# Kernel optimization log

Measured on AMD Instinct MI355X. Metric: run time of the kernel, lower is better.

The kernel has to match this reference:

```python
import jax, jax.numpy as jnp
import numpy as np


def setup_inputs() -> dict:
    key = jax.random.key(0)
    k1, k2 = jax.random.split(key)
    B, C, N = 8, 64, 65536
    features = jax.random.normal(k1, (B, C, N), dtype=jnp.float32)
    coords = jax.random.uniform(k2, (B, 3, N), dtype=jnp.float32)  # normalized xyz in [0,1)
    return {"features": features, "coords": coords, "resolution": 32}


def reference(features, coords, resolution):
    """avg_voxelize: quantize coords to an r^3 grid, scatter-average features.

    features: [B, C, N] float; coords: [B, 3, N] float in [0,1].
    Returns (vox [B, C, r, r, r], norm_coords [B, 3, N]).
    """
    r = resolution
    B, C, N = features.shape
    norm_coords = jnp.clip(coords * r, 0, r - 1)                 # [B, 3, N]
    vox = jnp.round(norm_coords).astype(jnp.int32)               # [B, 3, N]
    # linear voxel index per point: x*r^2 + y*r + z
    idx = (vox[:, 0] * r + vox[:, 1]) * r + vox[:, 2]            # [B, N]
    flat_idx = (idx + jnp.arange(B, dtype=jnp.int32)[:, None] * (r * r * r)).reshape(-1)  # [B*N]
    feats = features.transpose(0, 2, 1).reshape(B * N, C)        # [B*N, C]
    num_seg = B * r * r * r
    sums = jax.ops.segment_sum(feats, flat_idx, num_segments=num_seg)            # [B*r^3, C]
    cnt = jax.ops.segment_sum(jnp.ones((B * N,), features.dtype), flat_idx,
                              num_segments=num_seg)                              # [B*r^3]
    avg = sums / jnp.maximum(cnt, 1.0)[:, None]
    out = avg.reshape(B, r, r, r, C).transpose(0, 4, 1, 2, 3)    # [B, C, r, r, r]
    return out, norm_coords
```

## Files before the change

### kernel.cpp

```cpp
#include <hip/hip_runtime.h>
#include <hip/hip_bf16.h>


#define BB 8
#define CC 64
#define NN 65536
#define RR 32
#define R3 (RR * RR * RR)
#define OFFSTRIDE (R3 + 1)

__global__ __launch_bounds__(256) void points_kernel(
    const float* __restrict__ coords,
    float* __restrict__ norm_out,
    unsigned int* __restrict__ cnt,
    unsigned int* __restrict__ packed)
{
    int gid = blockIdx.x * 256 + threadIdx.x;
    int b = gid >> 16;
    int n = gid & (NN - 1);

    const float* cb = coords + (size_t)b * 3 * NN;
    float x = cb[n];
    float y = cb[NN + n];
    float z = cb[2 * NN + n];

    float nx = fminf(fmaxf(x * (float)RR, 0.0f), (float)(RR - 1));
    float ny = fminf(fmaxf(y * (float)RR, 0.0f), (float)(RR - 1));
    float nz = fminf(fmaxf(z * (float)RR, 0.0f), (float)(RR - 1));

    float* nb = norm_out + (size_t)b * 3 * NN;
    nb[n] = nx;
    nb[NN + n] = ny;
    nb[2 * NN + n] = nz;

    int vx = (int)rintf(nx);
    int vy = (int)rintf(ny);
    int vz = (int)rintf(nz);
    unsigned int idx = (unsigned int)((vx * RR + vy) * RR + vz);

    unsigned int rank = atomicAdd(&cnt[b * R3 + idx], 1u);
    packed[gid] = (idx << 17) | rank;
}

__global__ __launch_bounds__(1024) void scan_kernel(
    const unsigned int* __restrict__ cnt,
    unsigned int* __restrict__ off)
{
    int b = blockIdx.x;
    int t = threadIdx.x;
    const unsigned int* c = cnt + (size_t)b * R3;
    unsigned int* o = off + (size_t)b * OFFSTRIDE;

    unsigned int loc[32];
    unsigned int s = 0;
    #pragma unroll
    for (int k = 0; k < 32; k++) { loc[k] = c[t * 32 + k]; s += loc[k]; }

    __shared__ unsigned int aux[1024];
    aux[t] = s;
    __syncthreads();
    for (int d = 1; d < 1024; d <<= 1) {
        unsigned int v = (t >= d) ? aux[t - d] : 0u;
        __syncthreads();
        aux[t] += v;
        __syncthreads();
    }
    unsigned int run = (t == 0) ? 0u : aux[t - 1];
    #pragma unroll
    for (int k = 0; k < 32; k++) { o[t * 32 + k] = run; run += loc[k]; }
    if (t == 1023) o[R3] = run;
}

__global__ __launch_bounds__(256) void pos_kernel(
    const unsigned int* __restrict__ packed,
    const unsigned int* __restrict__ off,
    unsigned int* __restrict__ pos)
{
    int gid = blockIdx.x * 256 + threadIdx.x;
    int b = gid >> 16;
    unsigned int pk = packed[gid];
    unsigned int ix = pk >> 17;
    unsigned int rk = pk & 0x1FFFFu;
    pos[gid] = off[(size_t)b * OFFSTRIDE + ix] + rk;
}

__global__ __launch_bounds__(1024) void gather_kernel(
    const float* __restrict__ feats,
    const unsigned int* __restrict__ pos,
    const unsigned int* __restrict__ off,
    float* __restrict__ out)
{
    __shared__ __hip_bfloat16 srt[NN];

    int c = blockIdx.x;
    int b = blockIdx.y;
    int t = threadIdx.x;

    const float* f = feats + ((size_t)b * CC + c) * NN;
    const unsigned int* P = pos + (size_t)b * NN;

    for (int n0 = t * 4; n0 < NN; n0 += 1024 * 4) {
        float4 fv = *(const float4*)(f + n0);
        uint4 pv = *(const uint4*)(P + n0);
        srt[pv.x] = __float2bfloat16(fv.x);
        srt[pv.y] = __float2bfloat16(fv.y);
        srt[pv.z] = __float2bfloat16(fv.z);
        srt[pv.w] = __float2bfloat16(fv.w);
    }
    __syncthreads();

    const unsigned int* O = off + (size_t)b * OFFSTRIDE;
    float* ob = out + ((size_t)b * CC + c) * R3;
    for (int j = 0; j < 32; j++) {
        int v = t + j * 1024;
        unsigned int s0 = O[v];
        unsigned int s1 = O[v + 1];
        float s = 0.0f;
        for (unsigned int p = s0; p < s1; p++) s += __bfloat162float(srt[p]);
        float cf = (float)(s1 - s0);
        ob[v] = s / fmaxf(cf, 1.0f);
    }
}

extern "C" void kernel_launch(void* const* d_in, const int* in_sizes, int n_in,
                              void* d_out, int out_size, void* d_ws, size_t ws_size,
                              hipStream_t stream) {
    const float* feats  = (const float*)d_in[0];
    const float* coords = (const float*)d_in[1];

    float* out_vox  = (float*)d_out;
    float* out_norm = out_vox + (size_t)BB * CC * R3;

    char* ws = (char*)d_ws;
    unsigned int* cnt    = (unsigned int*)ws;
    unsigned int* off    = (unsigned int*)(ws + 1048576);
    unsigned int* packed = (unsigned int*)(ws + 1048576 + 1048608);
    unsigned int* pos    = (unsigned int*)(ws + 1048576 + 1048608 + 2097152);

    hipMemsetAsync(cnt, 0, (size_t)BB * R3 * sizeof(unsigned int), stream);

    points_kernel<<<(BB * NN) / 256, 256, 0, stream>>>(coords, out_norm, cnt, packed);
    scan_kernel<<<BB, 1024, 0, stream>>>(cnt, off);
    pos_kernel<<<(BB * NN) / 256, 256, 0, stream>>>(packed, off, pos);
    gather_kernel<<<dim3(CC, BB), 1024, 0, stream>>>(feats, pos, off, out_vox);
}
```

Measured before the change: 289.8 us.

## Pad atomic counters, split scan into multi-block passes, restructure gather segment loop

Spreads the per-voxel counters 16 words apart so that atomics on neighbouring voxels fall on different cache lines. The single-block-per-batch scan is replaced by a three-kernel chunked scan that uses wavefront shuffles across 256 blocks. The gather kernel now has each thread handle 32 consecutive voxels: it loads their offsets as vectors and walks the sorted bf16 values in one running pass. That pass uses 8-bit packed segment lengths and a hand-written bf16 conversion. The padded counter array is 16x larger, which makes the memset cost more, and there are two extra launches. The 8-bit length packing fails if a voxel receives 256 or more points.

After: 360.3 us. 1.24x slower.

```diff
diff --git a/kernel.cpp b/kernel.cpp
--- a/kernel.cpp
+++ b/kernel.cpp
@@ -1,13 +1,22 @@
 #include <hip/hip_runtime.h>
-#include <hip/hip_bf16.h>
 
 
 #define BB 8
 #define CC 64
 #define NN 65536
 #define RR 32
-#define R3 (RR * RR * RR)
-#define OFFSTRIDE (R3 + 1)
+#define R3 32768
+#define OFFPAD 32772
+#define CSTRIDE 16
+
+static __device__ inline unsigned short f2bf(float x) {
+    unsigned int u = __float_as_uint(x);
+    u += 0x7FFFu + ((u >> 16) & 1u);
+    return (unsigned short)(u >> 16);
+}
+static __device__ inline float bf2f(unsigned short h) {
+    return __uint_as_float((unsigned int)h << 16);
+}
 
 __global__ __launch_bounds__(256) void points_kernel(
     const float* __restrict__ coords,
@@ -38,37 +47,75 @@
     int vz = (int)rintf(nz);
     unsigned int idx = (unsigned int)((vx * RR + vy) * RR + vz);
 
-    unsigned int rank = atomicAdd(&cnt[b * R3 + idx], 1u);
+    unsigned int rank = atomicAdd(&cnt[(size_t)(b * R3 + idx) * CSTRIDE], 1u);
     packed[gid] = (idx << 17) | rank;
 }
 
-__global__ __launch_bounds__(1024) void scan_kernel(
+
+__global__ __launch_bounds__(256) void scan_a(
     const unsigned int* __restrict__ cnt,
-    unsigned int* __restrict__ off)
-{
-    int b = blockIdx.x;
-    int t = threadIdx.x;
-    const unsigned int* c = cnt + (size_t)b * R3;
-    unsigned int* o = off + (size_t)b * OFFSTRIDE;
-
-    unsigned int loc[32];
+    unsigned int* __restrict__ off,
+    unsigned int* __restrict__ chunksum)
+{
+    int blk = blockIdx.x;
+    int b = blk >> 5, chunk = blk & 31;
+    int t = threadIdx.x;
+    const unsigned int* c = cnt + ((size_t)b * R3 + chunk * 1024) * CSTRIDE;
+
+    unsigned int v[4];
     unsigned int s = 0;
     #pragma unroll
-    for (int k = 0; k < 32; k++) { loc[k] = c[t * 32 + k]; s += loc[k]; }
-
-    __shared__ unsigned int aux[1024];
-    aux[t] = s;
+    for (int k = 0; k < 4; k++) { v[k] = c[(size_t)(4 * t + k) * CSTRIDE]; s += v[k]; }
+
+    unsigned int incl = s;
+    #pragma unroll
+    for (int d = 1; d < 64; d <<= 1) {
+        unsigned int o = __shfl_up(incl, d, 64);
+        if ((t & 63) >= d) incl += o;
+    }
+    __shared__ unsigned int wsum[4];
+    int w = t >> 6;
+    if ((t & 63) == 63) wsum[w] = incl;
     __syncthreads();
-    for (int d = 1; d < 1024; d <<= 1) {
-        unsigned int v = (t >= d) ? aux[t - d] : 0u;
-        __syncthreads();
-        aux[t] += v;
-        __syncthreads();
-    }
-    unsigned int run = (t == 0) ? 0u : aux[t - 1];
-    #pragma unroll
-    for (int k = 0; k < 32; k++) { o[t * 32 + k] = run; run += loc[k]; }
-    if (t == 1023) o[R3] = run;
+    unsigned int woff = 0;
+    #pragma unroll
+    for (int i = 0; i < 3; i++) if (i < w) woff += wsum[i];
+
+    unsigned int run = woff + incl - s;
+    uint4 ov;
+    ov.x = run; run += v[0];
+    ov.y = run; run += v[1];
+    ov.z = run; run += v[2];
+    ov.w = run; run += v[3];
+    *(uint4*)(off + (size_t)b * OFFPAD + chunk * 1024 + 4 * t) = ov;
+    if (t == 255) chunksum[blk] = run;
+}
+
+__global__ __launch_bounds__(256) void scan_b(unsigned int* __restrict__ chunksum)
+{
+    int t = threadIdx.x;
+    unsigned int s = chunksum[t];
+    unsigned int incl = s;
+    #pragma unroll
+    for (int d = 1; d < 32; d <<= 1) {
+        unsigned int o = __shfl_up(incl, d, 32);
+        if ((t & 31) >= d) incl += o;
+    }
+    chunksum[t] = incl - s;
+}
+
+__global__ __launch_bounds__(256) void scan_c(
+    unsigned int* __restrict__ off, const unsigned int* __restrict__ chunksum)
+{
+    int blk = blockIdx.x;
+    int b = blk >> 5, chunk = blk & 31;
+    int t = threadIdx.x;
+    unsigned int add = chunksum[blk];
+    unsigned int* o = off + (size_t)b * OFFPAD + chunk * 1024 + 4 * t;
+    uint4 v = *(uint4*)o;
+    v.x += add; v.y += add; v.z += add; v.w += add;
+    *(uint4*)o = v;
+    if (chunk == 31 && t == 255) off[(size_t)b * OFFPAD + R3] = NN;
 }
 
 __global__ __launch_bounds__(256) void pos_kernel(
@@ -79,9 +126,7 @@
     int gid = blockIdx.x * 256 + threadIdx.x;
     int b = gid >> 16;
     unsigned int pk = packed[gid];
-    unsigned int ix = pk >> 17;
-    unsigned int rk = pk & 0x1FFFFu;
-    pos[gid] = off[(size_t)b * OFFSTRIDE + ix] + rk;
+    pos[gid] = off[(size_t)b * OFFPAD + (pk >> 17)] + (pk & 0x1FFFFu);
 }
 
 __global__ __launch_bounds__(1024) void gather_kernel(
@@ -90,7 +135,7 @@
     const unsigned int* __restrict__ off,
     float* __restrict__ out)
 {
-    __shared__ __hip_bfloat16 srt[NN];
+    __shared__ unsigned short srt[NN];
 
     int c = blockIdx.x;
     int b = blockIdx.y;
@@ -99,26 +144,59 @@
     const float* f = feats + ((size_t)b * CC + c) * NN;
     const unsigned int* P = pos + (size_t)b * NN;
 
-    for (int n0 = t * 4; n0 < NN; n0 += 1024 * 4) {
+    #pragma unroll
+    for (int it = 0; it < 16; it++) {
+        int n0 = t * 4 + it * 4096;
         float4 fv = *(const float4*)(f + n0);
         uint4 pv = *(const uint4*)(P + n0);
-        srt[pv.x] = __float2bfloat16(fv.x);
-        srt[pv.y] = __float2bfloat16(fv.y);
-        srt[pv.z] = __float2bfloat16(fv.z);
-        srt[pv.w] = __float2bfloat16(fv.w);
+        srt[pv.x] = f2bf(fv.x);
+        srt[pv.y] = f2bf(fv.y);
+        srt[pv.z] = f2bf(fv.z);
+        srt[pv.w] = f2bf(fv.w);
     }
     __syncthreads();
 
-    const unsigned int* O = off + (size_t)b * OFFSTRIDE;
-    float* ob = out + ((size_t)b * CC + c) * R3;
-    for (int j = 0; j < 32; j++) {
-        int v = t + j * 1024;
-        unsigned int s0 = O[v];
-        unsigned int s1 = O[v + 1];
+    const unsigned int* O = off + (size_t)b * OFFPAD + 32 * t;
+    unsigned int Ob[33];
+    #pragma unroll
+    for (int k = 0; k < 8; k++) {
+        uint4 u = *(const uint4*)(O + 4 * k);
+        Ob[4 * k + 0] = u.x; Ob[4 * k + 1] = u.y;
+        Ob[4 * k + 2] = u.z; Ob[4 * k + 3] = u.w;
+    }
+    Ob[32] = O[32];
+
+    float* ob = out + ((size_t)b * CC + c) * R3 + 32 * t;
+    unsigned int p = Ob[0];
+
+    #pragma unroll
+    for (int g = 0; g < 8; g++) {
+        unsigned int lw = 0;
+        #pragma unroll
+        for (int j = 0; j < 4; j++)
+            lw |= (Ob[4 * g + j + 1] - Ob[4 * g + j]) << (8 * j);
+        unsigned int eg = Ob[4 * g + 4];
+
+        int vj = 0;
+        unsigned int rem = lw & 255u;
+        unsigned int len = rem;
         float s = 0.0f;
-        for (unsigned int p = s0; p < s1; p++) s += __bfloat162float(srt[p]);
-        float cf = (float)(s1 - s0);
-        ob[v] = s / fmaxf(cf, 1.0f);
+        while (vj < 4 && rem == 0u) {
+            ob[4 * g + vj] = 0.0f;
+            vj++;
+            lw >>= 8; rem = lw & 255u; len = rem;
+        }
+        while (p < eg) {
+            s += bf2f(srt[p]);
+            p++;
+            rem--;
+            while (vj < 4 && rem == 0u) {
+                ob[4 * g + vj] = s / (float)max(len, 1u);
+                s = 0.0f;
+                vj++;
+                lw >>= 8; rem = lw & 255u; len = rem;
+            }
+        }
     }
 }
 
@@ -132,15 +210,22 @@
     float* out_norm = out_vox + (size_t)BB * CC * R3;
 
     char* ws = (char*)d_ws;
-    unsigned int* cnt    = (unsigned int*)ws;
-    unsigned int* off    = (unsigned int*)(ws + 1048576);
-    unsigned int* packed = (unsigned int*)(ws + 1048576 + 1048608);
-    unsigned int* pos    = (unsigned int*)(ws + 1048576 + 1048608 + 2097152);
-
-    hipMemsetAsync(cnt, 0, (size_t)BB * R3 * sizeof(unsigned int), stream);
+    const size_t CNT_B  = (size_t)BB * R3 * CSTRIDE * 4;
+    const size_t OFF_B  = (size_t)BB * OFFPAD * 4;
+    const size_t PK_B   = (size_t)BB * NN * 4;
+
+    unsigned int* cnt      = (unsigned int*)ws;
+    unsigned int* off      = (unsigned int*)(ws + CNT_B);
+    unsigned int* packed   = (unsigned int*)(ws + CNT_B + OFF_B);
+    unsigned int* pos      = (unsigned int*)(ws + CNT_B + OFF_B + PK_B);
+    unsigned int* chunksum = (unsigned int*)(ws + CNT_B + OFF_B + 2 * PK_B);
+
+    hipMemsetAsync(cnt, 0, CNT_B, stream);
 
     points_kernel<<<(BB * NN) / 256, 256, 0, stream>>>(coords, out_norm, cnt, packed);
-    scan_kernel<<<BB, 1024, 0, stream>>>(cnt, off);
+    scan_a<<<256, 256, 0, stream>>>(cnt, off, chunksum);
+    scan_b<<<1, 256, 0, stream>>>(chunksum);
+    scan_c<<<256, 256, 0, stream>>>(off, chunksum);
     pos_kernel<<<(BB * NN) / 256, 256, 0, stream>>>(packed, off, pos);
     gather_kernel<<<dim3(CC, BB), 1024, 0, stream>>>(feats, pos, off, out_vox);
 }
```
